# Kernel tuning notes

Measured on AMD Instinct MI355X. Metric: run time of the kernel, lower is better.

Reference implementation:

```python
import jax, jax.numpy as jnp
import numpy as np

INPUT_SIZE = 128
HIDDEN = 128
BATCH = 32
SEQ = 2048


def setup_inputs() -> dict:
    key = jax.random.key(0)
    k1, k2, k3, k4 = jax.random.split(key, 4)
    std = 1.0 / np.sqrt(HIDDEN)
    x = jax.random.normal(k1, (BATCH, SEQ, INPUT_SIZE), dtype=jnp.float32)
    Wi = jax.random.uniform(k2, (INPUT_SIZE, 4 * HIDDEN), minval=-std, maxval=std, dtype=jnp.float32)
    Wh = jax.random.uniform(k3, (HIDDEN, 4 * HIDDEN), minval=-std, maxval=std, dtype=jnp.float32)
    B = jax.random.uniform(k4, (4 * HIDDEN,), minval=-std, maxval=std, dtype=jnp.float32)
    return {"x": x, "Wi": Wi, "Wh": Wh, "B": B}


def _cell(xt, ht, ct, Wi, Wh, B, H):
    # gates: [bs, 4H] -> split into i, f, g, o
    gates = xt @ Wi + ht @ Wh + B
    i = jax.nn.sigmoid(gates[:, :H])
    f = jax.nn.sigmoid(gates[:, H:2 * H])
    g = jnp.tanh(gates[:, 2 * H:3 * H])
    o = jax.nn.sigmoid(gates[:, 3 * H:])
    ct = f * ct + i * g
    ht = o * jnp.tanh(ct)
    return ht, ct


def reference(x, Wi, Wh, B):
    bs, seqs, _ = x.shape
    H = Wi.shape[1] // 4
    z = jnp.zeros((bs, H), dtype=x.dtype)

    def step(carry, inputs):
        ht, ct, hinvt, cinvt = carry
        xt, xinvt = inputs
        ht, ct = _cell(xt, ht, ct, Wi, Wh, B, H)
        hinvt, cinvt = _cell(xinvt, hinvt, cinvt, Wi, Wh, B, H)
        return (ht, ct, hinvt, cinvt), (ht, hinvt)

    xs_fwd = jnp.swapaxes(x, 0, 1)               # [seq, bs, in]
    xs_bwd = jnp.swapaxes(x[:, ::-1, :], 0, 1)   # reversed sequence
    carry, (hs, hinvs) = jax.lax.scan(step, (z, z, z, z), (xs_fwd, xs_bwd))
    # [bs, seq, 2H]
    output = jnp.concatenate([jnp.swapaxes(hs, 0, 1), jnp.swapaxes(hinvs, 0, 1)], axis=2)
    return output, carry
```

## Files before the change

### kernel.cpp

```cpp
#include <hip/hip_runtime.h>

#define BATCHN 32
#define SEQN   2048
#define INSZ   128
#define HN     128
#define G4     512

#define OUT_MAIN ((size_t)BATCHN * SEQN * 2 * HN)

typedef float v2f __attribute__((ext_vector_type(2)));
typedef float v4f __attribute__((ext_vector_type(4)));

#define PKFMA(ACC, A, B)                                        \
  asm("v_pk_fma_f32 %0, %1, %2, %0" : "+v"(ACC) : "v"(A), "v"(B))

__device__ __forceinline__ float fast_rcp(float x) {
  return __builtin_amdgcn_rcpf(x);
}

__device__ __forceinline__ float qsum(float x) {
  x += __int_as_float(__builtin_amdgcn_update_dpp(
      0, __float_as_int(x), 0xB1, 0xF, 0xF, true));
  x += __int_as_float(__builtin_amdgcn_update_dpp(
      0, __float_as_int(x), 0x4E, 0xF, 0xF, true));
  return x;
}

template <int IMM>
__device__ __forceinline__ float qperm(float x) {
  return __int_as_float(__builtin_amdgcn_update_dpp(
      0, __float_as_int(x), IMM, 0xF, 0xF, true));
}

__global__ __launch_bounds__(256, 2) void precompute_xw(
    const float* __restrict__ x, const float* __restrict__ Wi,
    const float* __restrict__ B, float* __restrict__ XW) {
  __shared__ float As[INSZ][64];
  __shared__ float Bs[INSZ][64];

  const int tid = threadIdx.x;
  const int m0 = blockIdx.x * 64;
  const int n0 = blockIdx.y * 64;

  {
    const int row = tid & 63;
    const int k4b = tid >> 6;
    const float4* xs4 = (const float4*)(x + (size_t)(m0 + row) * INSZ);
#pragma unroll
    for (int it = 0; it < 8; it++) {
      const int k4 = k4b + (it << 2);
      float4 v = xs4[k4];
      As[k4 * 4 + 0][row] = v.x;
      As[k4 * 4 + 1][row] = v.y;
      As[k4 * 4 + 2][row] = v.z;
      As[k4 * 4 + 3][row] = v.w;
    }
  }
  {
    const int n4 = tid & 15;
    const int kb = tid >> 4;
#pragma unroll
    for (int it = 0; it < 8; it++) {
      const int k = kb + (it << 4);
      float4 v = *(const float4*)(Wi + (size_t)k * G4 + n0 + n4 * 4);
      *(float4*)&Bs[k][n4 * 4] = v;
    }
  }
  __syncthreads();

  const int tx = tid & 15;
  const int ty = tid >> 4;
  float4 acc0 = {0, 0, 0, 0}, acc1 = {0, 0, 0, 0};
  float4 acc2 = {0, 0, 0, 0}, acc3 = {0, 0, 0, 0};

#pragma unroll 8
  for (int k = 0; k < INSZ; k++) {
    const float4 a = *(const float4*)&As[k][ty * 4];
    const float4 bv = *(const float4*)&Bs[k][tx * 4];
    acc0.x += a.x * bv.x; acc0.y += a.x * bv.y; acc0.z += a.x * bv.z; acc0.w += a.x * bv.w;
    acc1.x += a.y * bv.x; acc1.y += a.y * bv.y; acc1.z += a.y * bv.z; acc1.w += a.y * bv.w;
    acc2.x += a.z * bv.x; acc2.y += a.z * bv.y; acc2.z += a.z * bv.z; acc2.w += a.z * bv.w;
    acc3.x += a.w * bv.x; acc3.y += a.w * bv.y; acc3.z += a.w * bv.z; acc3.w += a.w * bv.w;
  }

  const float4 bb = *(const float4*)(B + n0 + tx * 4);
  float* dst = XW + (size_t)(m0 + ty * 4) * G4 + n0 + tx * 4;
  float4 o;
  o.x = acc0.x + bb.x; o.y = acc0.y + bb.y; o.z = acc0.z + bb.z; o.w = acc0.w + bb.w;
  *(float4*)(dst + 0 * G4) = o;
  o.x = acc1.x + bb.x; o.y = acc1.y + bb.y; o.z = acc1.z + bb.z; o.w = acc1.w + bb.w;
  *(float4*)(dst + 1 * G4) = o;
  o.x = acc2.x + bb.x; o.y = acc2.y + bb.y; o.z = acc2.z + bb.z; o.w = acc2.w + bb.w;
  *(float4*)(dst + 2 * G4) = o;
  o.x = acc3.x + bb.x; o.y = acc3.y + bb.y; o.z = acc3.z + bb.z; o.w = acc3.w + bb.w;
  *(float4*)(dst + 3 * G4) = o;
}

__global__ __launch_bounds__(512, 1) void lstm_recur(
    const float* __restrict__ XW, const float* __restrict__ Wh,
    float* __restrict__ out) {
  const int tid = threadIdx.x;
  const int l   = tid & 63;
  const int w   = tid >> 6;
  const int kq  = l & 3;
  const int jl  = l >> 2;
  const int j   = w * 16 + jl;
  const int b   = blockIdx.x & 31;
  const int dir = blockIdx.x >> 5;

  __shared__ float hs[2][HN];

  v2f whp0[16], whp1[16], whp2[16], whp3[16];
#pragma unroll
  for (int i = 0; i < 8; i++) {
    const int ch = (i + 2 * kq) & 7;
    const int kb = kq * 32 + ch * 4;
#pragma unroll
    for (int p = 0; p < 2; p++) {
      const size_t r0 = (size_t)(kb + 2 * p + 0) * G4;
      const size_t r1 = (size_t)(kb + 2 * p + 1) * G4;
      whp0[2 * i + p] = (v2f){Wh[r0 + 0 * HN + j], Wh[r1 + 0 * HN + j]};
      whp1[2 * i + p] = (v2f){Wh[r0 + 1 * HN + j], Wh[r1 + 1 * HN + j]};
      whp2[2 * i + p] = (v2f){Wh[r0 + 2 * HN + j], Wh[r1 + 2 * HN + j]};
      whp3[2 * i + p] = (v2f){Wh[r0 + 3 * HN + j], Wh[r1 + 3 * HN + j]};
    }
  }

  const bool k0 = (kq == 0), k1 = (kq == 1), k2 = (kq == 2);
  const float xsc = k2 ? -2.0f : -1.0f;
  const float asc = k2 ? 2.0f : 1.0f;
  const float abi = k2 ? -1.0f : 0.0f;

  if (tid < HN) hs[0][tid] = 0.f;
  float c = 0.f, h = 0.f;
  __syncthreads();

  const float* xwp = XW + (size_t)b * SEQN * G4 + (size_t)kq * HN + j;
  float xwA = xwp[(size_t)(dir ? SEQN - 1 : 0) * G4];
  float xwB = xwp[(size_t)(dir ? SEQN - 2 : 1) * G4];

#define LSTM_STEP(S, PAR, XWREG)                                               \
  {                                                                            \
    const int tpf = ((S) + 2 < SEQN) ? (S) + 2 : SEQN - 1;                     \
    const float xw_pf = xwp[(size_t)(dir ? (SEQN - 1 - tpf) : tpf) * G4];      \
    v2f ac0 = {0.f, 0.f}, ac1 = {0.f, 0.f};                                    \
    v2f ac2 = {0.f, 0.f}, ac3 = {0.f, 0.f};                                    \
    _Pragma("unroll")                                                          \
    for (int i = 0; i < 8; i++) {                                              \
      const int ch = (i + 2 * kq) & 7;                                         \
      const v4f hv = *(const v4f*)&hs[PAR][kq * 32 + ch * 4];                  \
      const v2f hlo = __builtin_shufflevector(hv, hv, 0, 1);                   \
      const v2f hhi = __builtin_shufflevector(hv, hv, 2, 3);                   \
      PKFMA(ac0, hlo, whp0[2 * i]); PKFMA(ac0, hhi, whp0[2 * i + 1]);          \
      PKFMA(ac1, hlo, whp1[2 * i]); PKFMA(ac1, hhi, whp1[2 * i + 1]);          \
      PKFMA(ac2, hlo, whp2[2 * i]); PKFMA(ac2, hhi, whp2[2 * i + 1]);          \
      PKFMA(ac3, hlo, whp3[2 * i]); PKFMA(ac3, hhi, whp3[2 * i + 1]);          \
    }                                                                          \
    float a0 = ac0.x + ac0.y, a1 = ac1.x + ac1.y;                              \
    float a2 = ac2.x + ac2.y, a3 = ac3.x + ac3.y;                              \
    a0 = qsum(a0); a1 = qsum(a1); a2 = qsum(a2); a3 = qsum(a3);                \
    float sel = k0 ? a0 : (k1 ? a1 : (k2 ? a2 : a3));                          \
    sel += XWREG;                                                              \
    const float e   = __expf(sel * xsc);                                       \
    const float r   = fast_rcp(1.0f + e);                                      \
    const float act = r * asc + abi;                                           \
    const float iv = qperm<0x00>(act);                                         \
    const float fv = qperm<0x55>(act);                                         \
    const float gv = qperm<0xAA>(act);                                         \
    const float ov = qperm<0xFF>(act);                                         \
    c = fv * c + iv * gv;                                                      \
    const float e2 = __expf(-2.0f * c);                                        \
    const float th = 2.0f * fast_rcp(1.0f + e2) - 1.0f;                        \
    h = ov * th;                                                               \
    if (kq == 0) {                                                             \
      hs[(PAR) ^ 1][j] = h;                                                    \
      out[((size_t)b * SEQN + (S)) * (2 * HN) + (size_t)dir * HN + j] = h;     \
    }                                                                          \
    asm volatile("s_waitcnt lgkmcnt(0)" ::: "memory");                         \
    __builtin_amdgcn_s_barrier();                                              \
    XWREG = xw_pf;                                                             \
  }

  for (int s = 0; s < SEQN; s += 2) {
    LSTM_STEP(s, 0, xwA);
    LSTM_STEP(s + 1, 1, xwB);
  }
#undef LSTM_STEP

  if (kq == 0) {
    float* carry = out + OUT_MAIN;
    carry[(size_t)(dir * 2 + 0) * BATCHN * HN + (size_t)b * HN + j] = h;
    carry[(size_t)(dir * 2 + 1) * BATCHN * HN + (size_t)b * HN + j] = c;
  }
}

__global__ __launch_bounds__(512, 2) void lstm_recur_noxw(
    const float* __restrict__ x, const float* __restrict__ Wi,
    const float* __restrict__ Wh, const float* __restrict__ B,
    float* __restrict__ out) {
  const int j   = threadIdx.x;
  const int b   = blockIdx.x & 31;
  const int dir = blockIdx.x >> 5;

  __shared__ __align__(16) float hs[HN];
  __shared__ __align__(16) float xs[INSZ];
  __shared__ float gs[G4];

  float wh[HN];
#pragma unroll
  for (int k = 0; k < HN; k++) wh[k] = Wh[(size_t)k * G4 + j];
  const float bj = B[j];

  if (j < HN) hs[j] = 0.0f;
  float c = 0.0f, hlast = 0.0f;
  const int gtype = j >> 7;
  __syncthreads();

  for (int s = 0; s < SEQN; s++) {
    const int t = dir ? (SEQN - 1 - s) : s;
    if (j < INSZ / 4) {
      ((float4*)xs)[j] = ((const float4*)(x + ((size_t)b * SEQN + t) * INSZ))[j];
    }
    __syncthreads();

    float a0 = bj, a1 = 0.f, a2 = 0.f, a3 = 0.f;
    for (int k = 0; k < INSZ; k += 4) {
      a0 += xs[k + 0] * Wi[(size_t)(k + 0) * G4 + j] + hs[k + 0] * wh[k + 0];
      a1 += xs[k + 1] * Wi[(size_t)(k + 1) * G4 + j] + hs[k + 1] * wh[k + 1];
      a2 += xs[k + 2] * Wi[(size_t)(k + 2) * G4 + j] + hs[k + 2] * wh[k + 2];
      a3 += xs[k + 3] * Wi[(size_t)(k + 3) * G4 + j] + hs[k + 3] * wh[k + 3];
    }
    const float g = (a0 + a1) + (a2 + a3);

    float act;
    if (gtype == 2) act = 2.f * fast_rcp(1.f + __expf(-2.f * g)) - 1.f;
    else            act = fast_rcp(1.f + __expf(-g));
    gs[j] = act;
    __syncthreads();

    if (j < HN) {
      const float iv = gs[j];
      const float fv = gs[j + HN];
      const float gv = gs[j + 2 * HN];
      const float ov = gs[j + 3 * HN];
      c = fv * c + iv * gv;
      hlast = ov * (2.f * fast_rcp(1.f + __expf(-2.f * c)) - 1.f);
      hs[j] = hlast;
      out[((size_t)b * SEQN + s) * (2 * HN) + (size_t)dir * HN + j] = hlast;
    }
    __syncthreads();
  }

  if (j < HN) {
    float* carry = out + OUT_MAIN;
    carry[((size_t)(dir * 2 + 0)) * BATCHN * HN + (size_t)b * HN + j] = hlast;
    carry[((size_t)(dir * 2 + 1)) * BATCHN * HN + (size_t)b * HN + j] = c;
  }
}

extern "C" void kernel_launch(void* const* d_in, const int* in_sizes, int n_in,
                              void* d_out, int out_size, void* d_ws, size_t ws_size,
                              hipStream_t stream) {
  const float* x  = (const float*)d_in[0];
  const float* Wi = (const float*)d_in[1];
  const float* Wh = (const float*)d_in[2];
  const float* B  = (const float*)d_in[3];
  float* out = (float*)d_out;

  const size_t xw_bytes = (size_t)BATCHN * SEQN * G4 * sizeof(float);
  if (ws_size >= xw_bytes) {
    float* XW = (float*)d_ws;
    precompute_xw<<<dim3(1024, 8), dim3(256), 0, stream>>>(x, Wi, B, XW);
    lstm_recur<<<dim3(64), dim3(512), 0, stream>>>(XW, Wh, out);
  } else {
    lstm_recur_noxw<<<dim3(64), dim3(512), 0, stream>>>(x, Wi, Wh, B, out);
  }
}
```

Baseline: 1.227 ms.

## Split recurrent matvec K across two lanes instead of four, using 256 threads

Restructures the recurrent LSTM kernel so each hidden unit is handled by 2 lanes, each owning half of K (64), instead of 4 lanes with 32 each. The block shrinks from 512 to 256 threads (4 waves), the cross-lane reduction drops from two DPP steps to one, and each lane now evaluates two gate activations. The intent is to shorten the per-step serial chain and make the barrier cheaper. In exchange each lane keeps 128 weight registers and does twice the FMAs per step, which raises register pressure and per-step compute latency.

```diff
diff --git a/kernel.cpp b/kernel.cpp
--- a/kernel.cpp
+++ b/kernel.cpp
@@ -18,18 +18,9 @@
   return __builtin_amdgcn_rcpf(x);
 }
 
-__device__ __forceinline__ float qsum(float x) {
-  x += __int_as_float(__builtin_amdgcn_update_dpp(
+__device__ __forceinline__ float dppswap(float x) {
+  return __int_as_float(__builtin_amdgcn_update_dpp(
       0, __float_as_int(x), 0xB1, 0xF, 0xF, true));
-  x += __int_as_float(__builtin_amdgcn_update_dpp(
-      0, __float_as_int(x), 0x4E, 0xF, 0xF, true));
-  return x;
-}
-
-template <int IMM>
-__device__ __forceinline__ float qperm(float x) {
-  return __int_as_float(__builtin_amdgcn_update_dpp(
-      0, __float_as_int(x), IMM, 0xF, 0xF, true));
 }
 
 __global__ __launch_bounds__(256, 2) void precompute_xw(
@@ -96,98 +87,104 @@
   *(float4*)(dst + 3 * G4) = o;
 }
 
-__global__ __launch_bounds__(512, 1) void lstm_recur(
+__global__ __launch_bounds__(256, 1) void lstm_recur(
     const float* __restrict__ XW, const float* __restrict__ Wh,
     float* __restrict__ out) {
   const int tid = threadIdx.x;
+  const int w   = tid >> 6;
   const int l   = tid & 63;
-  const int w   = tid >> 6;
-  const int kq  = l & 3;
-  const int jl  = l >> 2;
-  const int j   = w * 16 + jl;
+  const int kh  = l & 1;
+  const int jl  = l >> 1;
+  const int j   = w * 32 + jl;
   const int b   = blockIdx.x & 31;
   const int dir = blockIdx.x >> 5;
 
   __shared__ float hs[2][HN];
 
-  v2f whp0[16], whp1[16], whp2[16], whp3[16];
-#pragma unroll
-  for (int i = 0; i < 8; i++) {
-    const int ch = (i + 2 * kq) & 7;
-    const int kb = kq * 32 + ch * 4;
+  v2f wA[32], wB[32], wC[32], wD[32];
+#pragma unroll
+  for (int i = 0; i < 16; i++) {
+    const int ch = (i + 8 * kh) & 15;
+    const int kb = kh * 64 + ch * 4;
 #pragma unroll
     for (int p = 0; p < 2; p++) {
       const size_t r0 = (size_t)(kb + 2 * p + 0) * G4;
       const size_t r1 = (size_t)(kb + 2 * p + 1) * G4;
-      whp0[2 * i + p] = (v2f){Wh[r0 + 0 * HN + j], Wh[r1 + 0 * HN + j]};
-      whp1[2 * i + p] = (v2f){Wh[r0 + 1 * HN + j], Wh[r1 + 1 * HN + j]};
-      whp2[2 * i + p] = (v2f){Wh[r0 + 2 * HN + j], Wh[r1 + 2 * HN + j]};
-      whp3[2 * i + p] = (v2f){Wh[r0 + 3 * HN + j], Wh[r1 + 3 * HN + j]};
-    }
-  }
-
-  const bool k0 = (kq == 0), k1 = (kq == 1), k2 = (kq == 2);
-  const float xsc = k2 ? -2.0f : -1.0f;
-  const float asc = k2 ? 2.0f : 1.0f;
-  const float abi = k2 ? -1.0f : 0.0f;
+      wA[2 * i + p] = (v2f){Wh[r0 + 0 * HN + j], Wh[r1 + 0 * HN + j]};
+      wB[2 * i + p] = (v2f){Wh[r0 + 1 * HN + j], Wh[r1 + 1 * HN + j]};
+      wC[2 * i + p] = (v2f){Wh[r0 + 2 * HN + j], Wh[r1 + 2 * HN + j]};
+      wD[2 * i + p] = (v2f){Wh[r0 + 3 * HN + j], Wh[r1 + 3 * HN + j]};
+    }
+  }
+
+  const bool kh1 = (kh == 1);
+  const float xscA = kh1 ? -2.0f : -1.0f;
+  const float ascA = kh1 ? 2.0f : 1.0f;
+  const float abiA = kh1 ? -1.0f : 0.0f;
 
   if (tid < HN) hs[0][tid] = 0.f;
   float c = 0.f, h = 0.f;
   __syncthreads();
 
-  const float* xwp = XW + (size_t)b * SEQN * G4 + (size_t)kq * HN + j;
-  float xwA = xwp[(size_t)(dir ? SEQN - 1 : 0) * G4];
-  float xwB = xwp[(size_t)(dir ? SEQN - 2 : 1) * G4];
-
-#define LSTM_STEP(S, PAR, XWREG)                                               \
+  const float* xwp = XW + (size_t)b * SEQN * G4 + (size_t)(2 * kh) * HN + j;
+  const size_t t0 = (size_t)(dir ? SEQN - 1 : 0) * G4;
+  const size_t t1 = (size_t)(dir ? SEQN - 2 : 1) * G4;
+  float xwA0 = xwp[t0], xwA1 = xwp[t0 + HN];
+  float xwB0 = xwp[t1], xwB1 = xwp[t1 + HN];
+
+#define LSTM_STEP(S, PAR, X0, X1)                                              \
   {                                                                            \
     const int tpf = ((S) + 2 < SEQN) ? (S) + 2 : SEQN - 1;                     \
-    const float xw_pf = xwp[(size_t)(dir ? (SEQN - 1 - tpf) : tpf) * G4];      \
+    const size_t tpo = (size_t)(dir ? (SEQN - 1 - tpf) : tpf) * G4;            \
+    const float pf0 = xwp[tpo];                                                \
+    const float pf1 = xwp[tpo + HN];                                           \
     v2f ac0 = {0.f, 0.f}, ac1 = {0.f, 0.f};                                    \
     v2f ac2 = {0.f, 0.f}, ac3 = {0.f, 0.f};                                    \
     _Pragma("unroll")                                                          \
-    for (int i = 0; i < 8; i++) {                                              \
-      const int ch = (i + 2 * kq) & 7;                                         \
-      const v4f hv = *(const v4f*)&hs[PAR][kq * 32 + ch * 4];                  \
+    for (int i = 0; i < 16; i++) {                                             \
+      const int ch = (i + 8 * kh) & 15;                                        \
+      const v4f hv = *(const v4f*)&hs[PAR][kh * 64 + ch * 4];                  \
       const v2f hlo = __builtin_shufflevector(hv, hv, 0, 1);                   \
       const v2f hhi = __builtin_shufflevector(hv, hv, 2, 3);                   \
-      PKFMA(ac0, hlo, whp0[2 * i]); PKFMA(ac0, hhi, whp0[2 * i + 1]);          \
-      PKFMA(ac1, hlo, whp1[2 * i]); PKFMA(ac1, hhi, whp1[2 * i + 1]);          \
-      PKFMA(ac2, hlo, whp2[2 * i]); PKFMA(ac2, hhi, whp2[2 * i + 1]);          \
-      PKFMA(ac3, hlo, whp3[2 * i]); PKFMA(ac3, hhi, whp3[2 * i + 1]);          \
+      PKFMA(ac0, hlo, wA[2 * i]); PKFMA(ac0, hhi, wA[2 * i + 1]);              \
+      PKFMA(ac1, hlo, wB[2 * i]); PKFMA(ac1, hhi, wB[2 * i + 1]);              \
+      PKFMA(ac2, hlo, wC[2 * i]); PKFMA(ac2, hhi, wC[2 * i + 1]);              \
+      PKFMA(ac3, hlo, wD[2 * i]); PKFMA(ac3, hhi, wD[2 * i + 1]);              \
     }                                                                          \
-    float a0 = ac0.x + ac0.y, a1 = ac1.x + ac1.y;                              \
-    float a2 = ac2.x + ac2.y, a3 = ac3.x + ac3.y;                              \
-    a0 = qsum(a0); a1 = qsum(a1); a2 = qsum(a2); a3 = qsum(a3);                \
-    float sel = k0 ? a0 : (k1 ? a1 : (k2 ? a2 : a3));                          \
-    sel += XWREG;                                                              \
-    const float e   = __expf(sel * xsc);                                       \
-    const float r   = fast_rcp(1.0f + e);                                      \
-    const float act = r * asc + abi;                                           \
-    const float iv = qperm<0x00>(act);                                         \
-    const float fv = qperm<0x55>(act);                                         \
-    const float gv = qperm<0xAA>(act);                                         \
-    const float ov = qperm<0xFF>(act);                                         \
+    float s0 = ac0.x + ac0.y, s1 = ac1.x + ac1.y;                              \
+    float s2 = ac2.x + ac2.y, s3 = ac3.x + ac3.y;                              \
+    s0 += dppswap(s0); s1 += dppswap(s1);                                      \
+    s2 += dppswap(s2); s3 += dppswap(s3);                                      \
+    float sA = (kh1 ? s2 : s0) + X0;                                           \
+    float sB = (kh1 ? s3 : s1) + X1;                                           \
+    const float actA = ascA * fast_rcp(1.0f + __expf(sA * xscA)) + abiA;       \
+    const float actB = fast_rcp(1.0f + __expf(-sB));                           \
+    const float pAo = dppswap(actA);                                           \
+    const float pBo = dppswap(actB);                                           \
+    const float iv = kh1 ? pAo : actA;                                         \
+    const float fv = kh1 ? pBo : actB;                                         \
+    const float gv = kh1 ? actA : pAo;                                         \
+    const float ov = kh1 ? actB : pBo;                                         \
     c = fv * c + iv * gv;                                                      \
-    const float e2 = __expf(-2.0f * c);                                        \
-    const float th = 2.0f * fast_rcp(1.0f + e2) - 1.0f;                        \
+    const float th = 2.0f * fast_rcp(1.0f + __expf(-2.0f * c)) - 1.0f;         \
     h = ov * th;                                                               \
-    if (kq == 0) {                                                             \
+    if (kh == 0) {                                                             \
       hs[(PAR) ^ 1][j] = h;                                                    \
       out[((size_t)b * SEQN + (S)) * (2 * HN) + (size_t)dir * HN + j] = h;     \
     }                                                                          \
     asm volatile("s_waitcnt lgkmcnt(0)" ::: "memory");                         \
     __builtin_amdgcn_s_barrier();                                              \
-    XWREG = xw_pf;                                                             \
-  }
-
+    X0 = pf0; X1 = pf1;                                                        \
+  }
+
+#pragma unroll 1
   for (int s = 0; s < SEQN; s += 2) {
-    LSTM_STEP(s, 0, xwA);
-    LSTM_STEP(s + 1, 1, xwB);
+    LSTM_STEP(s, 0, xwA0, xwA1);
+    LSTM_STEP(s + 1, 1, xwB0, xwB1);
   }
 #undef LSTM_STEP
 
-  if (kq == 0) {
+  if (kh == 0) {
     float* carry = out + OUT_MAIN;
     carry[(size_t)(dir * 2 + 0) * BATCHN * HN + (size_t)b * HN + j] = h;
     carry[(size_t)(dir * 2 + 1) * BATCHN * HN + (size_t)b * HN + j] = c;
@@ -271,7 +268,7 @@
   if (ws_size >= xw_bytes) {
     float* XW = (float*)d_ws;
     precompute_xw<<<dim3(1024, 8), dim3(256), 0, stream>>>(x, Wi, B, XW);
-    lstm_recur<<<dim3(64), dim3(512), 0, stream>>>(XW, Wh, out);
+    lstm_recur<<<dim3(64), dim3(256), 0, stream>>>(XW, Wh, out);
   } else {
     lstm_recur_noxw<<<dim3(64), dim3(512), 0, stream>>>(x, Wi, Wh, B, out);
   }
```

After: 2.221 ms. +81.1%, slower.

## Split LSTM recurrence K-reduction 8-way across 1024 threads; swap precompute grid axes

Applied to the files above, without the earlier changes.

The recurrent kernel moves from 512 to 1024 threads per block. Each hidden unit's dot product with Wh is now split over 8 lanes instead of 4, which halves the per-thread packed-FMA chain and register-held weights. The partial sums are combined with an extra row_half_mirror DPP step. The precompute GEMM grid is transposed so that consecutive blocks cover the N tiles of the same M rows, which may improve cache reuse of x. The cost is 16 waves joining every per-step barrier and one more cross-lane add on the serial critical path.

```diff
diff --git a/kernel.cpp b/kernel.cpp
--- a/kernel.cpp
+++ b/kernel.cpp
@@ -18,11 +18,13 @@
   return __builtin_amdgcn_rcpf(x);
 }
 
-__device__ __forceinline__ float qsum(float x) {
+__device__ __forceinline__ float redsum8(float x) {
   x += __int_as_float(__builtin_amdgcn_update_dpp(
       0, __float_as_int(x), 0xB1, 0xF, 0xF, true));
   x += __int_as_float(__builtin_amdgcn_update_dpp(
       0, __float_as_int(x), 0x4E, 0xF, 0xF, true));
+  x += __int_as_float(__builtin_amdgcn_update_dpp(
+      0, __float_as_int(x), 0x141, 0xF, 0xF, true));
   return x;
 }
 
@@ -39,8 +41,8 @@
   __shared__ float Bs[INSZ][64];
 
   const int tid = threadIdx.x;
-  const int m0 = blockIdx.x * 64;
-  const int n0 = blockIdx.y * 64;
+  const int m0 = blockIdx.y * 64;
+  const int n0 = blockIdx.x * 64;
 
   {
     const int row = tid & 63;
@@ -96,46 +98,44 @@
   *(float4*)(dst + 3 * G4) = o;
 }
 
-__global__ __launch_bounds__(512, 1) void lstm_recur(
+__global__ __launch_bounds__(1024) void lstm_recur2(
     const float* __restrict__ XW, const float* __restrict__ Wh,
     float* __restrict__ out) {
   const int tid = threadIdx.x;
-  const int l   = tid & 63;
-  const int w   = tid >> 6;
-  const int kq  = l & 3;
-  const int jl  = l >> 2;
-  const int j   = w * 16 + jl;
+  const int kg  = tid & 7;
+  const int j   = tid >> 3;
   const int b   = blockIdx.x & 31;
   const int dir = blockIdx.x >> 5;
 
   __shared__ float hs[2][HN];
 
-  v2f whp0[16], whp1[16], whp2[16], whp3[16];
-#pragma unroll
-  for (int i = 0; i < 8; i++) {
-    const int ch = (i + 2 * kq) & 7;
-    const int kb = kq * 32 + ch * 4;
+  v2f wg0[8], wg1[8], wg2[8], wg3[8];
+#pragma unroll
+  for (int c4 = 0; c4 < 4; c4++) {
+    const int sub = (((kg >> 1) + c4) & 3);
 #pragma unroll
     for (int p = 0; p < 2; p++) {
-      const size_t r0 = (size_t)(kb + 2 * p + 0) * G4;
-      const size_t r1 = (size_t)(kb + 2 * p + 1) * G4;
-      whp0[2 * i + p] = (v2f){Wh[r0 + 0 * HN + j], Wh[r1 + 0 * HN + j]};
-      whp1[2 * i + p] = (v2f){Wh[r0 + 1 * HN + j], Wh[r1 + 1 * HN + j]};
-      whp2[2 * i + p] = (v2f){Wh[r0 + 2 * HN + j], Wh[r1 + 2 * HN + j]};
-      whp3[2 * i + p] = (v2f){Wh[r0 + 3 * HN + j], Wh[r1 + 3 * HN + j]};
-    }
-  }
-
-  const bool k0 = (kq == 0), k1 = (kq == 1), k2 = (kq == 2);
-  const float xsc = k2 ? -2.0f : -1.0f;
-  const float asc = k2 ? 2.0f : 1.0f;
-  const float abi = k2 ? -1.0f : 0.0f;
+      const int k0 = kg * 16 + sub * 4 + 2 * p;
+      const size_t r0 = (size_t)k0 * G4;
+      const size_t r1 = (size_t)(k0 + 1) * G4;
+      wg0[c4 * 2 + p] = (v2f){Wh[r0 + 0 * HN + j], Wh[r1 + 0 * HN + j]};
+      wg1[c4 * 2 + p] = (v2f){Wh[r0 + 1 * HN + j], Wh[r1 + 1 * HN + j]};
+      wg2[c4 * 2 + p] = (v2f){Wh[r0 + 2 * HN + j], Wh[r1 + 2 * HN + j]};
+      wg3[c4 * 2 + p] = (v2f){Wh[r0 + 3 * HN + j], Wh[r1 + 3 * HN + j]};
+    }
+  }
+
+  const int gate = kg & 3;
+  const bool g0 = (gate == 0), g1 = (gate == 1), g2 = (gate == 2);
+  const float xsc = g2 ? -2.0f : -1.0f;
+  const float asc = g2 ? 2.0f : 1.0f;
+  const float abi = g2 ? -1.0f : 0.0f;
 
   if (tid < HN) hs[0][tid] = 0.f;
   float c = 0.f, h = 0.f;
   __syncthreads();
 
-  const float* xwp = XW + (size_t)b * SEQN * G4 + (size_t)kq * HN + j;
+  const float* xwp = XW + (size_t)b * SEQN * G4 + (size_t)gate * HN + j;
   float xwA = xwp[(size_t)(dir ? SEQN - 1 : 0) * G4];
   float xwB = xwp[(size_t)(dir ? SEQN - 2 : 1) * G4];
 
@@ -146,20 +146,21 @@
     v2f ac0 = {0.f, 0.f}, ac1 = {0.f, 0.f};                                    \
     v2f ac2 = {0.f, 0.f}, ac3 = {0.f, 0.f};                                    \
     _Pragma("unroll")                                                          \
-    for (int i = 0; i < 8; i++) {                                              \
-      const int ch = (i + 2 * kq) & 7;                                         \
-      const v4f hv = *(const v4f*)&hs[PAR][kq * 32 + ch * 4];                  \
+    for (int c4 = 0; c4 < 4; c4++) {                                           \
+      const int sub = (((kg >> 1) + c4) & 3);                                  \
+      const v4f hv = *(const v4f*)&hs[PAR][kg * 16 + sub * 4];                 \
       const v2f hlo = __builtin_shufflevector(hv, hv, 0, 1);                   \
       const v2f hhi = __builtin_shufflevector(hv, hv, 2, 3);                   \
-      PKFMA(ac0, hlo, whp0[2 * i]); PKFMA(ac0, hhi, whp0[2 * i + 1]);          \
-      PKFMA(ac1, hlo, whp1[2 * i]); PKFMA(ac1, hhi, whp1[2 * i + 1]);          \
-      PKFMA(ac2, hlo, whp2[2 * i]); PKFMA(ac2, hhi, whp2[2 * i + 1]);          \
-      PKFMA(ac3, hlo, whp3[2 * i]); PKFMA(ac3, hhi, whp3[2 * i + 1]);          \
+      PKFMA(ac0, hlo, wg0[c4 * 2]); PKFMA(ac0, hhi, wg0[c4 * 2 + 1]);          \
+      PKFMA(ac1, hlo, wg1[c4 * 2]); PKFMA(ac1, hhi, wg1[c4 * 2 + 1]);          \
+      PKFMA(ac2, hlo, wg2[c4 * 2]); PKFMA(ac2, hhi, wg2[c4 * 2 + 1]);          \
+      PKFMA(ac3, hlo, wg3[c4 * 2]); PKFMA(ac3, hhi, wg3[c4 * 2 + 1]);          \
     }                                                                          \
     float a0 = ac0.x + ac0.y, a1 = ac1.x + ac1.y;                              \
     float a2 = ac2.x + ac2.y, a3 = ac3.x + ac3.y;                              \
-    a0 = qsum(a0); a1 = qsum(a1); a2 = qsum(a2); a3 = qsum(a3);                \
-    float sel = k0 ? a0 : (k1 ? a1 : (k2 ? a2 : a3));                          \
+    a0 = redsum8(a0); a1 = redsum8(a1);                                        \
+    a2 = redsum8(a2); a3 = redsum8(a3);                                        \
+    float sel = g0 ? a0 : (g1 ? a1 : (g2 ? a2 : a3));                          \
     sel += XWREG;                                                              \
     const float e   = __expf(sel * xsc);                                       \
     const float r   = fast_rcp(1.0f + e);                                      \
@@ -172,7 +173,7 @@
     const float e2 = __expf(-2.0f * c);                                        \
     const float th = 2.0f * fast_rcp(1.0f + e2) - 1.0f;                        \
     h = ov * th;                                                               \
-    if (kq == 0) {                                                             \
+    if (kg == 0) {                                                             \
       hs[(PAR) ^ 1][j] = h;                                                    \
       out[((size_t)b * SEQN + (S)) * (2 * HN) + (size_t)dir * HN + j] = h;     \
     }                                                                          \
@@ -181,13 +182,14 @@
     XWREG = xw_pf;                                                             \
   }
 
+#pragma unroll 1
   for (int s = 0; s < SEQN; s += 2) {
     LSTM_STEP(s, 0, xwA);
     LSTM_STEP(s + 1, 1, xwB);
   }
 #undef LSTM_STEP
 
-  if (kq == 0) {
+  if (kg == 0) {
     float* carry = out + OUT_MAIN;
     carry[(size_t)(dir * 2 + 0) * BATCHN * HN + (size_t)b * HN + j] = h;
     carry[(size_t)(dir * 2 + 1) * BATCHN * HN + (size_t)b * HN + j] = c;
@@ -270,8 +272,8 @@
   const size_t xw_bytes = (size_t)BATCHN * SEQN * G4 * sizeof(float);
   if (ws_size >= xw_bytes) {
     float* XW = (float*)d_ws;
-    precompute_xw<<<dim3(1024, 8), dim3(256), 0, stream>>>(x, Wi, B, XW);
-    lstm_recur<<<dim3(64), dim3(512), 0, stream>>>(XW, Wh, out);
+    precompute_xw<<<dim3(8, 1024), dim3(256), 0, stream>>>(x, Wi, B, XW);
+    lstm_recur2<<<dim3(64), dim3(1024), 0, stream>>>(XW, Wh, out);
   } else {
     lstm_recur_noxw<<<dim3(64), dim3(512), 0, stream>>>(x, Wi, Wh, B, out);
   }
```

After: 1.547 ms. +26.1%, slower.
